# Performance work log

Hardware: AMD Instinct MI355X
Metric: run time of the kernel (lower is better)

The kernel has to match this reference:

```python
import jax, jax.numpy as jnp
import numpy as np

LMAX = 3
KMAX = [128, 96, 64, 32]   # k_max_l, decreasing in l
N_ATOMS = 10000
N_EDGES = 100000
N_RADIAL = 8
CUTOFF = 5.0

def _bounds(l):
    lo = KMAX[l + 1] if l < LMAX else 0
    return lo, KMAX[l]

def _uncouple(split_list, U):
    # split_list: per l' in 0..L, [n, 2l'+1, k]; U: [3**L, (L+1)**2]
    x = jnp.concatenate(split_list, axis=1)      # [n, (L+1)**2, k]
    return jnp.einsum('dm,nmk->ndk', U, x)       # [n, 3**L, k]

def _couple(f, U, L):
    x = jnp.einsum('dm,ndk->nmk', U, f)          # [n, (L+1)**2, k]
    out, off = [], 0
    for lp in range(L + 1):
        out.append(x[:, off:off + 2 * lp + 1, :])
        off += 2 * lp + 1
    return out

def _forward(r, sh, feat, Wrad, U, Wlin, centers, neighbors):
    # radial basis with smooth cutoff, then per-l channel embedding
    n = jnp.arange(1, N_RADIAL + 1, dtype=r.dtype)
    rb = jnp.sin(n * jnp.pi * r[:, None] / CUTOFF) / (r[:, None] + 1e-6)
    fc = 0.5 * (jnp.cos(jnp.pi * jnp.clip(r / CUTOFF, 0.0, 1.0)) + 1.0)
    rb = rb * fc[:, None]                        # [E, N_RADIAL]
    radial = [rb @ Wrad[l] for l in range(LMAX + 1)]          # [E, KMAX[l]]
    vexp = [sh[l] * radial[l][:, None, :] for l in range(LMAX + 1)]  # [E, 2l+1, KMAX[l]]

    def group(ts, l):
        lo, hi = _bounds(l)
        return [ts[lp][:, :, lo:hi] for lp in range(l + 1)]

    unc_v = [_uncouple(group(vexp, l), U[l]) for l in range(LMAX + 1)]
    unc_f = [_uncouple(group(feat, l), U[l]) for l in range(LMAX + 1)]
    # neighbor gather + elementwise combine in the uncoupled (Cartesian) space
    combined = [unc_v[l] * unc_f[l][neighbors] for l in range(LMAX + 1)]
    # scatter-add pooling over centers (index_add_ equivalent)
    pooled = [jax.ops.segment_sum(c, centers, num_segments=N_ATOMS) for c in combined]
    coupled = [_couple(pooled[l], U[l], l) for l in range(LMAX + 1)]
    cat = [jnp.concatenate([coupled[lp][l] for lp in range(l, LMAX + 1)], axis=-1)
           for l in range(LMAX + 1)]             # [n_atoms, 2l+1, KMAX[l]]
    # NOTE: mp_scaling multiply in the original is dead code (result unused)
    out = [feat[l] + jnp.einsum('nmk,kq->nmq', cat[l], Wlin[l]) for l in range(LMAX + 1)]
    return tuple(out)

def setup_inputs() -> dict:
    key = jax.random.key(0)
    ks = jax.random.split(key, 40)
    inp = {'r': jax.random.uniform(ks[0], (N_EDGES,), minval=0.5, maxval=CUTOFF, dtype=jnp.float32)}
    for l in range(LMAX + 1):
        k = KMAX[l]
        inp[f'sh{l}'] = jax.random.normal(ks[1 + l], (N_EDGES, 2 * l + 1, 1), dtype=jnp.float32)
        inp[f'feat{l}'] = jax.random.normal(ks[5 + l], (N_ATOMS, 2 * l + 1, k), dtype=jnp.float32)
        inp[f'Wrad{l}'] = jax.random.normal(ks[9 + l], (N_RADIAL, k), dtype=jnp.float32) / np.sqrt(N_RADIAL).astype(np.float32)
        inp[f'U{l}'] = jax.random.normal(ks[13 + l], (3 ** l, (l + 1) ** 2), dtype=jnp.float32) / np.float32(np.sqrt((l + 1) ** 2))
        inp[f'Wlin{l}'] = jax.random.normal(ks[17 + l], (k, k), dtype=jnp.float32) / np.sqrt(k).astype(np.float32)
    inp['centers'] = jax.random.randint(ks[21], (N_EDGES,), 0, N_ATOMS, dtype=jnp.int32)
    inp['neighbors'] = jax.random.randint(ks[22], (N_EDGES,), 0, N_ATOMS, dtype=jnp.int32)
    return inp

def reference(r, sh0, sh1, sh2, sh3, feat0, feat1, feat2, feat3,
              Wrad0, Wrad1, Wrad2, Wrad3, U0, U1, U2, U3,
              Wlin0, Wlin1, Wlin2, Wlin3, centers, neighbors):
    return _forward(r, [sh0, sh1, sh2, sh3], [feat0, feat1, feat2, feat3],
                    [Wrad0, Wrad1, Wrad2, Wrad3], [U0, U1, U2, U3],
                    [Wlin0, Wlin1, Wlin2, Wlin3], centers, neighbors)
```

## Files before the change

kernel.cpp:

```cpp
#include <hip/hip_runtime.h>
#include <hip/hip_fp16.h>
#include <math.h>

#define NA 10000
#define NE 100000
#define PI_F 3.14159265358979323846f


__device__ __forceinline__ constexpr int rowC(int row) {
    return (row == 0) ? 0 : (row < 4) ? 1 : (row < 13) ? 2 : 3;
}

__device__ __forceinline__ void stage_U(const float* __restrict__ U0,
                                        const float* __restrict__ U1,
                                        const float* __restrict__ U2,
                                        const float* __restrict__ U3,
                                        float* uLds, int t, int nthr) {
    for (int i = t; i < 526; i += nthr) {
        float v;
        if (i == 0)       v = U0[0];
        else if (i < 13)  v = U1[i - 1];
        else if (i < 94)  v = U2[i - 13];
        else              v = U3[i - 94];
        uLds[i] = v;
    }
}

__global__ __launch_bounds__(256) void kCount(const int* __restrict__ centers,
                                              int* __restrict__ counts)
{
    const int e = blockIdx.x * 256 + threadIdx.x;
    if (e < NE) atomicAdd(&counts[centers[e]], 1);
}

__global__ __launch_bounds__(1024) void kScan(const int* __restrict__ counts,
                                              int* __restrict__ offsets,
                                              int* __restrict__ cursor)
{
    __shared__ int sums[1024];
    const int t = threadIdx.x;
    const int base = t * 10;
    int local[10];
    int s = 0;
#pragma unroll
    for (int j = 0; j < 10; ++j) {
        int idx = base + j;
        int v = (idx < NA) ? counts[idx] : 0;
        local[j] = s;
        s += v;
    }
    sums[t] = s;
    __syncthreads();
    for (int off = 1; off < 1024; off <<= 1) {
        int v = (t >= off) ? sums[t - off] : 0;
        __syncthreads();
        sums[t] += v;
        __syncthreads();
    }
    const int prev = (t == 0) ? 0 : sums[t - 1];
#pragma unroll
    for (int j = 0; j < 10; ++j) {
        int idx = base + j;
        if (idx <= NA) {
            int o = prev + local[j];
            offsets[idx] = o;
            if (idx < NA) cursor[idx] = o;
        }
    }
}

__global__ __launch_bounds__(256) void kPrep(
    const float* __restrict__ f0, const float* __restrict__ f1,
    const float* __restrict__ f2, const float* __restrict__ f3,
    const float* __restrict__ r,
    const float* __restrict__ sh0, const float* __restrict__ sh1,
    const float* __restrict__ sh2, const float* __restrict__ sh3,
    const float* __restrict__ U0, const float* __restrict__ U1,
    const float* __restrict__ U2, const float* __restrict__ U3,
    const int* __restrict__ centers, const int* __restrict__ neighbors,
    int* __restrict__ cursor,
    uint4* __restrict__ uncf16, float* __restrict__ rbbuf,
    float* __restrict__ csbuf, int* __restrict__ nbrs)
{
    __shared__ float uLds[526];
    const int t = threadIdx.x;
    stage_U(U0, U1, U2, U3, uLds, t, 256);
    __syncthreads();

    if (blockIdx.x < 1250) {
        const int la = t >> 5, k = t & 31;
        const int a = blockIdx.x * 8 + la;
        float arr[40];

        {
            arr[0] = uLds[0] * f0[(size_t)a * 128 + 96 + k];
        }
        {
            float x[4];
            x[0] = f0[(size_t)a * 128 + 64 + k];
#pragma unroll
            for (int m = 0; m < 3; ++m) x[1 + m] = f1[(size_t)a * 288 + m * 96 + 64 + k];
#pragma unroll
            for (int d = 0; d < 3; ++d) {
                float acc = 0.f;
#pragma unroll
                for (int m = 0; m < 4; ++m) acc += uLds[1 + d * 4 + m] * x[m];
                arr[1 + d] = acc;
            }
        }
        {
            float x[9];
            x[0] = f0[(size_t)a * 128 + 32 + k];
#pragma unroll
            for (int m = 0; m < 3; ++m) x[1 + m] = f1[(size_t)a * 288 + m * 96 + 32 + k];
#pragma unroll
            for (int m = 0; m < 5; ++m) x[4 + m] = f2[(size_t)a * 320 + m * 64 + 32 + k];
#pragma unroll
            for (int d = 0; d < 9; ++d) {
                float acc = 0.f;
#pragma unroll
                for (int m = 0; m < 9; ++m) acc += uLds[13 + d * 9 + m] * x[m];
                arr[4 + d] = acc;
            }
        }
        {
            float x[16];
            x[0] = f0[(size_t)a * 128 + k];
#pragma unroll
            for (int m = 0; m < 3; ++m) x[1 + m] = f1[(size_t)a * 288 + m * 96 + k];
#pragma unroll
            for (int m = 0; m < 5; ++m) x[4 + m] = f2[(size_t)a * 320 + m * 64 + k];
#pragma unroll
            for (int m = 0; m < 7; ++m) x[9 + m] = f3[(size_t)a * 224 + m * 32 + k];
#pragma unroll
            for (int d = 0; d < 27; ++d) {
                float acc = 0.f;
#pragma unroll
                for (int m = 0; m < 16; ++m) acc += uLds[94 + d * 16 + m] * x[m];
                arr[13 + d] = acc;
            }
        }
        uint4* op = uncf16 + (size_t)a * 160 + k;
#pragma unroll
        for (int jj = 0; jj < 5; ++jj) {
            uint4 w;
            __half2 h0 = __floats2half2_rn(arr[8 * jj + 0], arr[8 * jj + 1]);
            __half2 h1 = __floats2half2_rn(arr[8 * jj + 2], arr[8 * jj + 3]);
            __half2 h2 = __floats2half2_rn(arr[8 * jj + 4], arr[8 * jj + 5]);
            __half2 h3 = __floats2half2_rn(arr[8 * jj + 6], arr[8 * jj + 7]);
            w.x = *(unsigned int*)&h0; w.y = *(unsigned int*)&h1;
            w.z = *(unsigned int*)&h2; w.w = *(unsigned int*)&h3;
            op[jj * 32] = w;
        }
    } else {
        const int e = (blockIdx.x - 1250) * 256 + t;
        if (e >= NE) return;

        const int c_ = centers[e];
        const int pos = atomicAdd(&cursor[c_], 1);
        nbrs[pos] = neighbors[e];

        float shv[16];
        shv[0] = sh0[e];
#pragma unroll
        for (int m = 0; m < 3; ++m) shv[1 + m] = sh1[(size_t)e * 3 + m];
#pragma unroll
        for (int m = 0; m < 5; ++m) shv[4 + m] = sh2[(size_t)e * 5 + m];
#pragma unroll
        for (int m = 0; m < 7; ++m) shv[9 + m] = sh3[(size_t)e * 7 + m];

        const float rv = r[e];
        const float fc = 0.5f * (cosf(PI_F * fminf(rv * 0.2f, 1.0f)) + 1.0f);
        const float pref = fc / (rv + 1e-6f);
        const float step = rv * (PI_F * 0.2f);
        float4 ra, rb;
        ra.x = sinf(1.f * step) * pref; ra.y = sinf(2.f * step) * pref;
        ra.z = sinf(3.f * step) * pref; ra.w = sinf(4.f * step) * pref;
        rb.x = sinf(5.f * step) * pref; rb.y = sinf(6.f * step) * pref;
        rb.z = sinf(7.f * step) * pref; rb.w = sinf(8.f * step) * pref;
        *(float4*)(rbbuf + (size_t)pos * 8)     = ra;
        *(float4*)(rbbuf + (size_t)pos * 8 + 4) = rb;

        const int UO[4] = {0, 1, 13, 94};
        const int RO[4] = {0, 1, 4, 13};
        const int P3[4] = {1, 3, 9, 27};
        float4* cso = (float4*)csbuf + (size_t)pos * 40;
#pragma unroll
        for (int c = 0; c < 4; ++c) {
            const int M2 = (c + 1) * (c + 1);
            for (int d = 0; d < P3[c]; ++d) {
                float4 cv = make_float4(0.f, 0.f, 0.f, 0.f);
                float* cvp = &cv.x;
#pragma unroll
                for (int lp = 0; lp < 4; ++lp) {
                    if (lp > c) break;
                    float s = 0.f;
#pragma unroll
                    for (int ml = 0; ml < 2 * lp + 1; ++ml)
                        s += uLds[UO[c] + d * M2 + lp * lp + ml] * shv[lp * lp + ml];
                    cvp[lp] = s;
                }
                cso[RO[c] + d] = cv;
            }
        }
    }
}

__global__ __launch_bounds__(256, 2) void kB2(
    const float* __restrict__ Wr0, const float* __restrict__ Wr1,
    const float* __restrict__ Wr2, const float* __restrict__ Wr3,
    const int* __restrict__ offsets, const int* __restrict__ nbrs,
    const float* __restrict__ rbbuf, const float* __restrict__ csbuf,
    const uint4* __restrict__ uncf16, float* __restrict__ pooled)
{
    __shared__ float wLds[2560];
    const int t = threadIdx.x;
    for (int i = t; i < 2560; i += 256) {
        float v;
        if (i < 1024)      v = Wr0[i];
        else if (i < 1792) v = Wr1[i - 1024];
        else if (i < 2304) v = Wr2[i - 1792];
        else               v = Wr3[i - 2304];
        wLds[i] = v;
    }
    __syncthreads();

    const int lane = t & 63;
    const int wv = t >> 6;
    const int k = lane & 31;
    const int g2 = lane >> 5;
    const int a = blockIdx.x * 4 + wv;
    const int beg = offsets[a], end = offsets[a + 1];

    float acc[40];
#pragma unroll
    for (int i = 0; i < 40; ++i) acc[i] = 0.f;

    const int KL[4] = {128, 96, 64, 32};
    const int WO[4] = {0, 1024, 1792, 2304};

    int i = beg + g2;
    int nbr = (i < end) ? nbrs[i] : 0;
    for (; i < end; i += 2) {
        const int nbr_nx = (i + 2 < end) ? nbrs[i + 2] : 0;

        const uint4* up = uncf16 + (size_t)nbr * 160 + k;
        const uint4 w0 = up[0 * 32];
        const uint4 w1 = up[1 * 32];
        const uint4 w2 = up[2 * 32];
        const uint4 w3 = up[3 * 32];
        const uint4 w4 = up[4 * 32];

        const float4 r0 = *(const float4*)(rbbuf + (size_t)i * 8);
        const float4 r1 = *(const float4*)(rbbuf + (size_t)i * 8 + 4);
        const float rb[8] = {r0.x, r0.y, r0.z, r0.w, r1.x, r1.y, r1.z, r1.w};

        float rad[4][4];
#pragma unroll
        for (int lp = 0; lp < 4; ++lp) {
#pragma unroll
            for (int c = 0; c < 4; ++c) {
                if (c < lp) continue;
                const int base = 32 * (3 - c);
                float s = 0.f;
#pragma unroll
                for (int n = 0; n < 8; ++n)
                    s += rb[n] * wLds[WO[lp] + n * KL[lp] + base + k];
                rad[lp][c] = s;
            }
        }

        const float4* cs = (const float4*)csbuf + (size_t)i * 40;
        const uint4 ww[5] = {w0, w1, w2, w3, w4};
#pragma unroll
        for (int jj = 0; jj < 5; ++jj) {
            const unsigned int ws[4] = {ww[jj].x, ww[jj].y, ww[jj].z, ww[jj].w};
#pragma unroll
            for (int p2 = 0; p2 < 4; ++p2) {
                const int row0 = 8 * jj + 2 * p2, row1 = row0 + 1;
                const int c0 = rowC(row0), c1 = rowC(row1);
                const __half2 h = *(const __half2*)&ws[p2];
                const float4 cva = cs[row0];
                const float4 cvb = cs[row1];
                float uv0 = cva.x * rad[0][c0];
                if (c0 >= 1) uv0 += cva.y * rad[1][c0];
                if (c0 >= 2) uv0 += cva.z * rad[2][c0];
                if (c0 >= 3) uv0 += cva.w * rad[3][c0];
                float uv1 = cvb.x * rad[0][c1];
                if (c1 >= 1) uv1 += cvb.y * rad[1][c1];
                if (c1 >= 2) uv1 += cvb.z * rad[2][c1];
                if (c1 >= 3) uv1 += cvb.w * rad[3][c1];
                acc[row0] += uv0 * __low2float(h);
                acc[row1] += uv1 * __high2float(h);
            }
        }
        nbr = nbr_nx;
    }

#pragma unroll
    for (int row = 0; row < 40; ++row) acc[row] += __shfl_xor(acc[row], 32);

    float* pp = pooled + (size_t)a * 1280 + k;
#pragma unroll
    for (int rr = 0; rr < 20; ++rr) {
        const float v   = g2 ? acc[rr + 20] : acc[rr];
        const int  row  = g2 ? (rr + 20)    : rr;
        pp[row * 32] = v;
    }
}

__global__ __launch_bounds__(256) void kC_out(
    const float* __restrict__ pooled,
    const float* __restrict__ f0, const float* __restrict__ f1,
    const float* __restrict__ f2, const float* __restrict__ f3,
    const float* __restrict__ U0, const float* __restrict__ U1,
    const float* __restrict__ U2, const float* __restrict__ U3,
    const float* __restrict__ W0, const float* __restrict__ W1,
    const float* __restrict__ W2, const float* __restrict__ W3,
    float* __restrict__ out)
{
    __shared__ float uLds[526];
    __shared__ float plds[4 * 1280];
    __shared__ float clds[4 * 960];
    const int t = threadIdx.x;
    stage_U(U0, U1, U2, U3, uLds, t, 256);
    const int a0 = blockIdx.x * 4;
    for (int i = t; i < 5120; i += 256) plds[i] = pooled[(size_t)a0 * 1280 + i];
    __syncthreads();

    for (int idx = t; idx < 3840; idx += 256) {
        const int la = idx / 960;
        const int rem = idx - la * 960;
        int c, off;
        if (rem < 32)       { c = 0; off = 0; }
        else if (rem < 160) { c = 1; off = 32; }
        else if (rem < 448) { c = 2; off = 160; }
        else                { c = 3; off = 448; }
        const int r2 = rem - off;
        const int m = r2 >> 5, k = r2 & 31;
        const int M2 = (c + 1) * (c + 1);
        const int UOc = (c == 0 ? 0 : c == 1 ? 1 : c == 2 ? 13 : 94);
        const int ROc = (c == 0 ? 0 : c == 1 ? 1 : c == 2 ? 4 : 13);
        const int nd  = (c == 0 ? 1 : c == 1 ? 3 : c == 2 ? 9 : 27);
        float acc = 0.f;
        for (int d = 0; d < nd; ++d)
            acc += uLds[UOc + d * M2 + m] * plds[la * 1280 + (ROc + d) * 32 + k];
        clds[idx] = acc;
    }
    __syncthreads();

    int l, m, q;
    bool active = true;
    if (t < 32)       { l = 0; m = 0;                               q = 4 * t; }
    else if (t < 104) { l = 1; int u = t - 32;  m = u / 24; q = 4 * (u % 24); }
    else if (t < 184) { l = 2; int u = t - 104; m = u / 16; q = 4 * (u % 16); }
    else if (t < 240) { l = 3; int u = t - 184; m = u / 8;  q = 4 * (u % 8);  }
    else active = false;

    if (active) {
        const int K  = (l == 0) ? 128 : (l == 1) ? 96 : (l == 2) ? 64 : 32;
        const int MK = (l == 0) ? 128 : (l == 1) ? 288 : (l == 2) ? 320 : 224;
        const size_t Ol = (l == 0) ? 0 : (l == 1) ? 1280000 : (l == 2) ? 4160000 : 7360000;
        const float* F = (l == 0) ? f0 : (l == 1) ? f1 : (l == 2) ? f2 : f3;
        const float* W = (l == 0) ? W0 : (l == 1) ? W1 : (l == 2) ? W2 : W3;
        const int CO[4] = {0, 32, 160, 448};

        float4 acc[4];
#pragma unroll
        for (int la = 0; la < 4; ++la)
            acc[la] = *(const float4*)(F + (size_t)(a0 + la) * MK + m * K + q);

        for (int j = 0; j < 4 - l; ++j) {
            const int c = l + j;
            const int cb = CO[c] + (l * l + m) * 32;
#pragma unroll
            for (int k = 0; k < 32; ++k) {
                const float4 w = *(const float4*)(W + (size_t)(32 * j + k) * K + q);
#pragma unroll
                for (int la = 0; la < 4; ++la) {
                    const float cv = clds[la * 960 + cb + k];
                    acc[la].x += cv * w.x; acc[la].y += cv * w.y;
                    acc[la].z += cv * w.z; acc[la].w += cv * w.w;
                }
            }
        }
#pragma unroll
        for (int la = 0; la < 4; ++la)
            *(float4*)(out + Ol + (size_t)(a0 + la) * MK + m * K + q) = acc[la];
    }
}

extern "C" void kernel_launch(void* const* d_in, const int* in_sizes, int n_in,
                              void* d_out, int out_size, void* d_ws, size_t ws_size,
                              hipStream_t stream)
{
    int ir, ish[4], ift[4], iwr[4], iu[4], iwl[4], ic, in_;
    if (in_sizes[2] == 300000) {
        ir = 0;
        for (int l = 0; l < 4; ++l) { ish[l] = 1 + l; ift[l] = 5 + l; iwr[l] = 9 + l; iu[l] = 13 + l; iwl[l] = 17 + l; }
        ic = 21; in_ = 22;
    } else {
        ir = 0;
        for (int l = 0; l < 4; ++l) { ish[l] = 1 + 5 * l; ift[l] = 2 + 5 * l; iwr[l] = 3 + 5 * l; iu[l] = 4 + 5 * l; iwl[l] = 5 + 5 * l; }
        ic = 21; in_ = 22;
    }
    const float* r   = (const float*)d_in[ir];
    const float* sh0 = (const float*)d_in[ish[0]];
    const float* sh1 = (const float*)d_in[ish[1]];
    const float* sh2 = (const float*)d_in[ish[2]];
    const float* sh3 = (const float*)d_in[ish[3]];
    const float* f0  = (const float*)d_in[ift[0]];
    const float* f1  = (const float*)d_in[ift[1]];
    const float* f2  = (const float*)d_in[ift[2]];
    const float* f3  = (const float*)d_in[ift[3]];
    const float* Wr0 = (const float*)d_in[iwr[0]];
    const float* Wr1 = (const float*)d_in[iwr[1]];
    const float* Wr2 = (const float*)d_in[iwr[2]];
    const float* Wr3 = (const float*)d_in[iwr[3]];
    const float* U0  = (const float*)d_in[iu[0]];
    const float* U1  = (const float*)d_in[iu[1]];
    const float* U2  = (const float*)d_in[iu[2]];
    const float* U3  = (const float*)d_in[iu[3]];
    const float* Wl0 = (const float*)d_in[iwl[0]];
    const float* Wl1 = (const float*)d_in[iwl[1]];
    const float* Wl2 = (const float*)d_in[iwl[2]];
    const float* Wl3 = (const float*)d_in[iwl[3]];
    const int* centers   = (const int*)d_in[ic];
    const int* neighbors = (const int*)d_in[in_];

    uint4* uncf16 = (uint4*)d_ws;
    float* pooled = (float*)(uncf16 + (size_t)NA * 160);
    float* rbbuf  = pooled + (size_t)NA * 1280;
    float* csbuf  = rbbuf + (size_t)NE * 8;
    int*   nbrs    = (int*)(csbuf + (size_t)NE * 160);
    int*   counts  = nbrs + NE;
    int*   offsets = counts + NA;
    int*   cursor  = offsets + NA + 1;
    float* outp   = (float*)d_out;

    hipMemsetAsync(counts, 0, NA * sizeof(int), stream);
    kCount<<<(NE + 255) / 256, 256, 0, stream>>>(centers, counts);
    kScan<<<1, 1024, 0, stream>>>(counts, offsets, cursor);
    kPrep<<<1250 + (NE + 255) / 256, 256, 0, stream>>>(
        f0, f1, f2, f3, r, sh0, sh1, sh2, sh3, U0, U1, U2, U3,
        centers, neighbors, cursor, uncf16, rbbuf, csbuf, nbrs);
    kB2<<<NA / 4, 256, 0, stream>>>(Wr0, Wr1, Wr2, Wr3, offsets, nbrs,
                                    rbbuf, csbuf, uncf16, pooled);
    kC_out<<<NA / 4, 256, 0, stream>>>(pooled, f0, f1, f2, f3, U0, U1, U2, U3,
                                       Wl0, Wl1, Wl2, Wl3, outp);
}
```

Measured before the change: 393.3 us.

## Fuse gather-pool kernel with coupling and output linear kernel

Merges the edge-gather/pooling kernel and the coupling plus linear output kernel into one launch. Each block keeps its four atoms' pooled accumulators in LDS instead of writing them to a global buffer and reading them back. This removes one launch and a global round trip for the pooled tensor. In exchange, LDS per block grows by about 36 KB on top of the existing 10 KB, which may lower occupancy under the 2-blocks-per-SM launch bound.

After: 436.8 us. +11.1%, slower.

```diff
diff --git a/kernel.cpp b/kernel.cpp
--- a/kernel.cpp
+++ b/kernel.cpp
@@ -206,14 +206,24 @@
     }
 }
 
-__global__ __launch_bounds__(256, 2) void kB2(
+__global__ __launch_bounds__(256, 2) void kBC(
     const float* __restrict__ Wr0, const float* __restrict__ Wr1,
     const float* __restrict__ Wr2, const float* __restrict__ Wr3,
     const int* __restrict__ offsets, const int* __restrict__ nbrs,
     const float* __restrict__ rbbuf, const float* __restrict__ csbuf,
-    const uint4* __restrict__ uncf16, float* __restrict__ pooled)
+    const uint4* __restrict__ uncf16,
+    const float* __restrict__ f0, const float* __restrict__ f1,
+    const float* __restrict__ f2, const float* __restrict__ f3,
+    const float* __restrict__ U0, const float* __restrict__ U1,
+    const float* __restrict__ U2, const float* __restrict__ U3,
+    const float* __restrict__ W0, const float* __restrict__ W1,
+    const float* __restrict__ W2, const float* __restrict__ W3,
+    float* __restrict__ out)
 {
     __shared__ float wLds[2560];
+    __shared__ float uLds[526];
+    __shared__ float plds[4 * 1280];
+    __shared__ float clds[4 * 960];
     const int t = threadIdx.x;
     for (int i = t; i < 2560; i += 256) {
         float v;
@@ -223,13 +233,15 @@
         else               v = Wr3[i - 2304];
         wLds[i] = v;
     }
+    stage_U(U0, U1, U2, U3, uLds, t, 256);
     __syncthreads();
 
     const int lane = t & 63;
     const int wv = t >> 6;
     const int k = lane & 31;
     const int g2 = lane >> 5;
-    const int a = blockIdx.x * 4 + wv;
+    const int a0 = blockIdx.x * 4;
+    const int a = a0 + wv;
     const int beg = offsets[a], end = offsets[a + 1];
 
     float acc[40];
@@ -300,32 +312,15 @@
 #pragma unroll
     for (int row = 0; row < 40; ++row) acc[row] += __shfl_xor(acc[row], 32);
 
-    float* pp = pooled + (size_t)a * 1280 + k;
-#pragma unroll
-    for (int rr = 0; rr < 20; ++rr) {
-        const float v   = g2 ? acc[rr + 20] : acc[rr];
-        const int  row  = g2 ? (rr + 20)    : rr;
-        pp[row * 32] = v;
-    }
-}
-
-__global__ __launch_bounds__(256) void kC_out(
-    const float* __restrict__ pooled,
-    const float* __restrict__ f0, const float* __restrict__ f1,
-    const float* __restrict__ f2, const float* __restrict__ f3,
-    const float* __restrict__ U0, const float* __restrict__ U1,
-    const float* __restrict__ U2, const float* __restrict__ U3,
-    const float* __restrict__ W0, const float* __restrict__ W1,
-    const float* __restrict__ W2, const float* __restrict__ W3,
-    float* __restrict__ out)
-{
-    __shared__ float uLds[526];
-    __shared__ float plds[4 * 1280];
-    __shared__ float clds[4 * 960];
-    const int t = threadIdx.x;
-    stage_U(U0, U1, U2, U3, uLds, t, 256);
-    const int a0 = blockIdx.x * 4;
-    for (int i = t; i < 5120; i += 256) plds[i] = pooled[(size_t)a0 * 1280 + i];
+    {
+        float* pp = plds + wv * 1280 + k;
+#pragma unroll
+        for (int rr = 0; rr < 20; ++rr) {
+            const float v  = g2 ? acc[rr + 20] : acc[rr];
+            const int  row = g2 ? (rr + 20)    : rr;
+            pp[row * 32] = v;
+        }
+    }
     __syncthreads();
 
     for (int idx = t; idx < 3840; idx += 256) {
@@ -337,15 +332,15 @@
         else if (rem < 448) { c = 2; off = 160; }
         else                { c = 3; off = 448; }
         const int r2 = rem - off;
-        const int m = r2 >> 5, k = r2 & 31;
+        const int m = r2 >> 5, kk = r2 & 31;
         const int M2 = (c + 1) * (c + 1);
         const int UOc = (c == 0 ? 0 : c == 1 ? 1 : c == 2 ? 13 : 94);
         const int ROc = (c == 0 ? 0 : c == 1 ? 1 : c == 2 ? 4 : 13);
         const int nd  = (c == 0 ? 1 : c == 1 ? 3 : c == 2 ? 9 : 27);
-        float acc = 0.f;
+        float accv = 0.f;
         for (int d = 0; d < nd; ++d)
-            acc += uLds[UOc + d * M2 + m] * plds[la * 1280 + (ROc + d) * 32 + k];
-        clds[idx] = acc;
+            accv += uLds[UOc + d * M2 + m] * plds[la * 1280 + (ROc + d) * 32 + kk];
+        clds[idx] = accv;
     }
     __syncthreads();
 
@@ -365,28 +360,28 @@
         const float* W = (l == 0) ? W0 : (l == 1) ? W1 : (l == 2) ? W2 : W3;
         const int CO[4] = {0, 32, 160, 448};
 
-        float4 acc[4];
+        float4 accv[4];
 #pragma unroll
         for (int la = 0; la < 4; ++la)
-            acc[la] = *(const float4*)(F + (size_t)(a0 + la) * MK + m * K + q);
+            accv[la] = *(const float4*)(F + (size_t)(a0 + la) * MK + m * K + q);
 
         for (int j = 0; j < 4 - l; ++j) {
             const int c = l + j;
             const int cb = CO[c] + (l * l + m) * 32;
 #pragma unroll
-            for (int k = 0; k < 32; ++k) {
-                const float4 w = *(const float4*)(W + (size_t)(32 * j + k) * K + q);
+            for (int kk = 0; kk < 32; ++kk) {
+                const float4 w = *(const float4*)(W + (size_t)(32 * j + kk) * K + q);
 #pragma unroll
                 for (int la = 0; la < 4; ++la) {
-                    const float cv = clds[la * 960 + cb + k];
-                    acc[la].x += cv * w.x; acc[la].y += cv * w.y;
-                    acc[la].z += cv * w.z; acc[la].w += cv * w.w;
+                    const float cv = clds[la * 960 + cb + kk];
+                    accv[la].x += cv * w.x; accv[la].y += cv * w.y;
+                    accv[la].z += cv * w.z; accv[la].w += cv * w.w;
                 }
             }
         }
 #pragma unroll
         for (int la = 0; la < 4; ++la)
-            *(float4*)(out + Ol + (size_t)(a0 + la) * MK + m * K + q) = acc[la];
+            *(float4*)(out + Ol + (size_t)(a0 + la) * MK + m * K + q) = accv[la];
     }
 }
 
@@ -429,8 +424,7 @@
     const int* neighbors = (const int*)d_in[in_];
 
     uint4* uncf16 = (uint4*)d_ws;
-    float* pooled = (float*)(uncf16 + (size_t)NA * 160);
-    float* rbbuf  = pooled + (size_t)NA * 1280;
+    float* rbbuf  = (float*)(uncf16 + (size_t)NA * 160);
     float* csbuf  = rbbuf + (size_t)NE * 8;
     int*   nbrs    = (int*)(csbuf + (size_t)NE * 160);
     int*   counts  = nbrs + NE;
@@ -444,8 +438,8 @@
     kPrep<<<1250 + (NE + 255) / 256, 256, 0, stream>>>(
         f0, f1, f2, f3, r, sh0, sh1, sh2, sh3, U0, U1, U2, U3,
         centers, neighbors, cursor, uncf16, rbbuf, csbuf, nbrs);
-    kB2<<<NA / 4, 256, 0, stream>>>(Wr0, Wr1, Wr2, Wr3, offsets, nbrs,
-                                    rbbuf, csbuf, uncf16, pooled);
-    kC_out<<<NA / 4, 256, 0, stream>>>(pooled, f0, f1, f2, f3, U0, U1, U2, U3,
-                                       Wl0, Wl1, Wl2, Wl3, outp);
-}
+    kBC<<<NA / 4, 256, 0, stream>>>(Wr0, Wr1, Wr2, Wr3, offsets, nbrs,
+                                    rbbuf, csbuf, uncf16,
+                                    f0, f1, f2, f3, U0, U1, U2, U3,
+                                    Wl0, Wl1, Wl2, Wl3, outp);
+}
```
